# Kernel optimization log

Hardware: AMD Instinct MI355X
Metric: run time of the kernel (lower is better)

The kernel has to match this reference:

```python
import jax, jax.numpy as jnp
import numpy as np

B, H, W, C = 128, 56, 56, 96
N = H * W  # tokens


def setup_inputs() -> dict:
    key = jax.random.key(0)
    k1, k2 = jax.random.split(key)
    x = jax.random.normal(k1, (B, N, C), dtype=jnp.float32)
    # original inits to 0.02 * ones; use small random values for a non-trivial baseline
    weight_c = jax.random.uniform(k2, (N, C // 2 + 1, 2), dtype=jnp.float32) * 0.02
    return {"x": x, "weight_c": weight_c}


def reference(x, weight_c):
    # x: [B, N, C]; rfft along channel dim, per-token complex filter, irfft back
    c = x.shape[2]
    xf = jnp.fft.rfft(x.astype(jnp.float32), axis=2, norm="ortho")  # [B, N, C//2+1] complex
    w = jax.lax.complex(weight_c[..., 0], weight_c[..., 1])          # [N, C//2+1] complex
    y = xf * w  # broadcast over batch
    return jnp.fft.irfft(y, n=c, axis=2, norm="ortho")  # [B, N, C]
```

## Files before the change

kernel.cpp:

```cpp
#include <hip/hip_runtime.h>
#include <hip/hip_bf16.h>

#ifndef M_PI
#define M_PI 3.14159265358979323846
#endif

static constexpr int B_ = 128;
static constexpr int N_ = 3136;
static constexpr int C_ = 96;
static constexpr int PITCH = 104;

typedef short short8 __attribute__((ext_vector_type(8)));
typedef float float4v __attribute__((ext_vector_type(4)));

static __device__ __forceinline__ unsigned short f2bf(float f) {
  __hip_bfloat16 b = __float2bfloat16(f);
  return *reinterpret_cast<unsigned short*>(&b);
}

__global__ __launch_bounds__(256, 3) void gf_mfma_kernel(
    const float* __restrict__ x, const float* __restrict__ wc,
    float* __restrict__ y) {
  const int n = blockIdx.x;
  const int tid = threadIdx.x;

  __shared__ __align__(16) unsigned short Asm[128 * PITCH];
  __shared__ __align__(16) unsigned short Ht[96 * PITCH];
  __shared__ float wsh[98];
  __shared__ float cs[96];
  __shared__ float sn[96];
  __shared__ unsigned short hrevd[192];

  float4 xv[12];
  const float* xbase = x + (size_t)n * C_;
#pragma unroll
  for (int p = 0; p < 12; ++p) {
    const int fidx = p * 256 + tid;
    const int b = fidx / 24;
    const int t4 = fidx - b * 24;
    xv[p] = *reinterpret_cast<const float4*>(xbase + (size_t)b * (N_ * C_) + 4 * t4);
  }

  if (tid < 98) wsh[tid] = wc[n * 98 + tid];
  if (tid < 96) {
    float s, c;
    sincosf((float)(2.0 * M_PI / 96.0) * (float)tid, &s, &c);
    cs[tid] = c;
    sn[tid] = s;
  }
  __syncthreads();

  if (tid < 96) {
    const int c = tid;
    float acc = wsh[0] + ((c & 1) ? -wsh[96] : wsh[96]);
    int idx = c;
    for (int k = 1; k <= 47; ++k) {
      acc += 2.0f * (wsh[2 * k] * cs[idx] - wsh[2 * k + 1] * sn[idx]);
      idx += c;
      if (idx >= 96) idx -= 96;
    }
    const unsigned short hb = f2bf(acc * (1.0f / 96.0f));
    hrevd[96 - c] = hb;
    hrevd[(c == 0) ? 0 : (192 - c)] = hb;
  }

#pragma unroll
  for (int p = 0; p < 12; ++p) {
    const int fidx = p * 256 + tid;
    const int b = fidx / 24;
    const int t4 = fidx - b * 24;
    ushort4 o;
    o.x = f2bf(xv[p].x);
    o.y = f2bf(xv[p].y);
    o.z = f2bf(xv[p].z);
    o.w = f2bf(xv[p].w);
    *reinterpret_cast<ushort4*>(&Asm[b * PITCH + 4 * t4]) = o;
  }
  __syncthreads();

  for (int j = tid; j < 96 * 48; j += 256) {
    const int c = j / 48;
    const int kp = j - c * 48;
    const int m = 96 - c + 2 * kp;
    const unsigned int lo = hrevd[m];
    const unsigned int hi = hrevd[m + 1];
    *reinterpret_cast<unsigned int*>(&Ht[c * PITCH + 2 * kp]) = lo | (hi << 16);
  }
  __syncthreads();

  const int wv = tid >> 6;
  const int l = tid & 63;
  const int lrow = l & 15;
  const int lk = l >> 4;

  float4v acc[2][6];
#pragma unroll
  for (int mt = 0; mt < 2; ++mt)
#pragma unroll
    for (int nt = 0; nt < 6; ++nt)
#pragma unroll
      for (int i = 0; i < 4; ++i) acc[mt][nt][i] = 0.0f;

  short8 afr[2][3];
#pragma unroll
  for (int mt = 0; mt < 2; ++mt)
#pragma unroll
    for (int kq = 0; kq < 3; ++kq)
      afr[mt][kq] = *reinterpret_cast<const short8*>(
          &Asm[((wv * 2 + mt) * 16 + lrow) * PITCH + kq * 32 + lk * 8]);

#pragma unroll
  for (int nt = 0; nt < 6; ++nt) {
#pragma unroll
    for (int kq = 0; kq < 3; ++kq) {
      const short8 bfr = *reinterpret_cast<const short8*>(
          &Ht[(nt * 16 + lrow) * PITCH + kq * 32 + lk * 8]);
      acc[0][nt] = __builtin_amdgcn_mfma_f32_16x16x32_bf16(afr[0][kq], bfr, acc[0][nt], 0, 0, 0);
      acc[1][nt] = __builtin_amdgcn_mfma_f32_16x16x32_bf16(afr[1][kq], bfr, acc[1][nt], 0, 0, 0);
    }
  }

#pragma unroll
  for (int mt = 0; mt < 2; ++mt) {
    const int brow0 = (wv * 2 + mt) * 16 + lk * 4;
#pragma unroll
    for (int i = 0; i < 4; ++i) {
      float* yp = y + (size_t)(brow0 + i) * (N_ * C_) + (size_t)n * C_;
#pragma unroll
      for (int nt = 0; nt < 6; ++nt) {
        yp[nt * 16 + lrow] = acc[mt][nt][i];
      }
    }
  }
}

extern "C" void kernel_launch(void* const* d_in, const int* in_sizes, int n_in,
                              void* d_out, int out_size, void* d_ws, size_t ws_size,
                              hipStream_t stream) {
  const float* x = (const float*)d_in[0];
  const float* wc = (const float*)d_in[1];
  float* y = (float*)d_out;

  hipLaunchKernelGGL(gf_mfma_kernel, dim3(N_), dim3(256), 0, stream, x, wc, y);
}
```

Baseline: 284.7 us.

## Split circulant filter build into prepass kernel and drop LDS staging from GEMM

A separate kernel computes each token's bf16 circulant filter once and writes it to workspace in eight shifted copies, so the main kernel can read MFMA B fragments straight from global memory with aligned 16-byte loads. The main kernel also loads x directly into A fragments in registers instead of staging through shared memory. This removes the LDS traffic, the barriers and the per-block sincos/DFT work, and raises the occupancy hint to 4. In exchange it adds a second launch and about 9.6 MB of workspace traffic, and the old path is kept as a fallback when the workspace is too small.

```diff
diff --git a/kernel.cpp b/kernel.cpp
--- a/kernel.cpp
+++ b/kernel.cpp
@@ -8,6 +8,7 @@
 static constexpr int B_ = 128;
 static constexpr int N_ = 3136;
 static constexpr int C_ = 96;
+static constexpr int NC = N_ * C_;
 static constexpr int PITCH = 104;
 
 typedef short short8 __attribute__((ext_vector_type(8)));
@@ -16,6 +17,124 @@
 static __device__ __forceinline__ unsigned short f2bf(float f) {
   __hip_bfloat16 b = __float2bfloat16(f);
   return *reinterpret_cast<unsigned short*>(&b);
+}
+
+__global__ __launch_bounds__(128) void gf_hbuild_kernel(
+    const float* __restrict__ wc, unsigned short* __restrict__ wsB) {
+  const int n = blockIdx.x;
+  const int tid = threadIdx.x;
+  __shared__ float wsh[98];
+  __shared__ float cs[96], sn[96];
+  __shared__ unsigned short hlb[96];
+
+  if (tid < 98) wsh[tid] = wc[n * 98 + tid];
+  if (tid < 96) {
+    float s, c;
+    sincosf((float)(2.0 * M_PI / 96.0) * (float)tid, &s, &c);
+    cs[tid] = c;
+    sn[tid] = s;
+  }
+  __syncthreads();
+
+  if (tid < 96) {
+    const int c = tid;
+    float acc = wsh[0] + ((c & 1) ? -wsh[96] : wsh[96]);
+    int idx = c;
+    for (int k = 1; k <= 47; ++k) {
+      acc += 2.0f * (wsh[2 * k] * cs[idx] - wsh[2 * k + 1] * sn[idx]);
+      idx += c;
+      if (idx >= 96) idx -= 96;
+    }
+    hlb[c] = f2bf(acc * (1.0f / 96.0f));
+  }
+  __syncthreads();
+
+  unsigned int* out = reinterpret_cast<unsigned int*>(wsB + (size_t)n * 1536);
+  for (int e = tid; e < 768; e += 128) {
+    const int s = e / 96;
+    const int jp = e - s * 96;
+    const int a = 288 - (2 * jp + s);
+    const unsigned int lo = hlb[a % 96];
+    const unsigned int hi = hlb[(a - 1) % 96];
+    out[e] = lo | (hi << 16);
+  }
+}
+
+__global__ __launch_bounds__(256, 4) void gf_mfma2_kernel(
+    const float* __restrict__ x, const unsigned short* __restrict__ wsB,
+    float* __restrict__ y) {
+  const int n = blockIdx.x;
+  const int tid = threadIdx.x;
+  const int wv = tid >> 6;
+  const int l = tid & 63;
+  const int lrow = l & 15;
+  const int lk = l >> 4;
+
+  float4 v0[2][3], v1[2][3];
+#pragma unroll
+  for (int mt = 0; mt < 2; ++mt) {
+    const float* xp =
+        x + (size_t)((wv * 2 + mt) * 16 + lrow) * NC + n * C_ + lk * 8;
+#pragma unroll
+    for (int kq = 0; kq < 3; ++kq) {
+      v0[mt][kq] = *reinterpret_cast<const float4*>(xp + kq * 32);
+      v1[mt][kq] = *reinterpret_cast<const float4*>(xp + kq * 32 + 4);
+    }
+  }
+  short8 afr[2][3];
+#pragma unroll
+  for (int mt = 0; mt < 2; ++mt)
+#pragma unroll
+    for (int kq = 0; kq < 3; ++kq) {
+      short8 a;
+      a[0] = (short)f2bf(v0[mt][kq].x);
+      a[1] = (short)f2bf(v0[mt][kq].y);
+      a[2] = (short)f2bf(v0[mt][kq].z);
+      a[3] = (short)f2bf(v0[mt][kq].w);
+      a[4] = (short)f2bf(v1[mt][kq].x);
+      a[5] = (short)f2bf(v1[mt][kq].y);
+      a[6] = (short)f2bf(v1[mt][kq].z);
+      a[7] = (short)f2bf(v1[mt][kq].w);
+      afr[mt][kq] = a;
+    }
+
+  const int M0 = 96 + lk * 8 - lrow;
+  const unsigned short* wb0 =
+      wsB + (size_t)n * 1536 + (M0 & 7) * 192 + (M0 & ~7);
+
+  float4v acc[2][6];
+#pragma unroll
+  for (int mt = 0; mt < 2; ++mt)
+#pragma unroll
+    for (int nt = 0; nt < 6; ++nt)
+#pragma unroll
+      for (int i = 0; i < 4; ++i) acc[mt][nt][i] = 0.0f;
+
+#pragma unroll
+  for (int nt = 0; nt < 6; ++nt) {
+#pragma unroll
+    for (int kq = 0; kq < 3; ++kq) {
+      const short8 bfr =
+          *reinterpret_cast<const short8*>(wb0 + kq * 32 - nt * 16);
+      acc[0][nt] = __builtin_amdgcn_mfma_f32_16x16x32_bf16(afr[0][kq], bfr,
+                                                           acc[0][nt], 0, 0, 0);
+      acc[1][nt] = __builtin_amdgcn_mfma_f32_16x16x32_bf16(afr[1][kq], bfr,
+                                                           acc[1][nt], 0, 0, 0);
+    }
+  }
+
+#pragma unroll
+  for (int mt = 0; mt < 2; ++mt) {
+    const int brow0 = (wv * 2 + mt) * 16 + lk * 4;
+#pragma unroll
+    for (int i = 0; i < 4; ++i) {
+      float* yp = y + (size_t)(brow0 + i) * NC + (size_t)n * C_;
+#pragma unroll
+      for (int nt = 0; nt < 6; ++nt) {
+        yp[nt * 16 + lrow] = acc[mt][nt][i];
+      }
+    }
+  }
 }
 
 __global__ __launch_bounds__(256, 3) void gf_mfma_kernel(
@@ -38,7 +157,7 @@
     const int fidx = p * 256 + tid;
     const int b = fidx / 24;
     const int t4 = fidx - b * 24;
-    xv[p] = *reinterpret_cast<const float4*>(xbase + (size_t)b * (N_ * C_) + 4 * t4);
+    xv[p] = *reinterpret_cast<const float4*>(xbase + (size_t)b * NC + 4 * t4);
   }
 
   if (tid < 98) wsh[tid] = wc[n * 98 + tid];
@@ -115,8 +234,10 @@
     for (int kq = 0; kq < 3; ++kq) {
       const short8 bfr = *reinterpret_cast<const short8*>(
           &Ht[(nt * 16 + lrow) * PITCH + kq * 32 + lk * 8]);
-      acc[0][nt] = __builtin_amdgcn_mfma_f32_16x16x32_bf16(afr[0][kq], bfr, acc[0][nt], 0, 0, 0);
-      acc[1][nt] = __builtin_amdgcn_mfma_f32_16x16x32_bf16(afr[1][kq], bfr, acc[1][nt], 0, 0, 0);
+      acc[0][nt] = __builtin_amdgcn_mfma_f32_16x16x32_bf16(afr[0][kq], bfr,
+                                                           acc[0][nt], 0, 0, 0);
+      acc[1][nt] = __builtin_amdgcn_mfma_f32_16x16x32_bf16(afr[1][kq], bfr,
+                                                           acc[1][nt], 0, 0, 0);
     }
   }
 
@@ -125,7 +246,7 @@
     const int brow0 = (wv * 2 + mt) * 16 + lk * 4;
 #pragma unroll
     for (int i = 0; i < 4; ++i) {
-      float* yp = y + (size_t)(brow0 + i) * (N_ * C_) + (size_t)n * C_;
+      float* yp = y + (size_t)(brow0 + i) * NC + (size_t)n * C_;
 #pragma unroll
       for (int nt = 0; nt < 6; ++nt) {
         yp[nt * 16 + lrow] = acc[mt][nt][i];
@@ -141,5 +262,12 @@
   const float* wc = (const float*)d_in[1];
   float* y = (float*)d_out;
 
-  hipLaunchKernelGGL(gf_mfma_kernel, dim3(N_), dim3(256), 0, stream, x, wc, y);
-}
+  const size_t need = (size_t)N_ * 1536 * sizeof(unsigned short);
+  if (ws_size >= need) {
+    unsigned short* wsB = (unsigned short*)d_ws;
+    hipLaunchKernelGGL(gf_hbuild_kernel, dim3(N_), dim3(128), 0, stream, wc, wsB);
+    hipLaunchKernelGGL(gf_mfma2_kernel, dim3(N_), dim3(256), 0, stream, x, wsB, y);
+  } else {
+    hipLaunchKernelGGL(gf_mfma_kernel, dim3(N_), dim3(256), 0, stream, x, wc, y);
+  }
+}
```

After: 298.5 us. 4.8% more time.

## Load x straight into MFMA fragments and read circulant filter from compact replicated table

Applied to the files above, without the earlier changes.

Each lane now loads x directly into its MFMA operand layout and converts to bf16 in registers, which removes the shared-memory staging of x. Operands are swapped so the circulant filter is the A operand and x is B. The filter is read from a small 8-way shifted replica table instead of a materialized 96x96 matrix. Output becomes contiguous float4 stores per lane, and the filter DFT is split across 192 threads. Shared memory drops sharply, so occupancy is raised to 4 blocks per SM. The risks are more scattered global loads for x and harder-to-verify index arithmetic.

```diff
diff --git a/kernel.cpp b/kernel.cpp
--- a/kernel.cpp
+++ b/kernel.cpp
@@ -8,7 +8,7 @@
 static constexpr int B_ = 128;
 static constexpr int N_ = 3136;
 static constexpr int C_ = 96;
-static constexpr int PITCH = 104;
+static constexpr int NC = N_ * C_;
 
 typedef short short8 __attribute__((ext_vector_type(8)));
 typedef float float4v __attribute__((ext_vector_type(4)));
@@ -18,27 +18,35 @@
   return *reinterpret_cast<unsigned short*>(&b);
 }
 
-__global__ __launch_bounds__(256, 3) void gf_mfma_kernel(
+static __device__ __forceinline__ int mod96(int a) {
+  return a >= 192 ? a - 192 : (a >= 96 ? a - 96 : a);
+}
+
+__global__ __launch_bounds__(256, 4) void gf_fused_kernel(
     const float* __restrict__ x, const float* __restrict__ wc,
     float* __restrict__ y) {
   const int n = blockIdx.x;
   const int tid = threadIdx.x;
+  const int wv = tid >> 6;
+  const int l = tid & 63;
+  const int lrow = l & 15;
+  const int lk = l >> 4;
 
-  __shared__ __align__(16) unsigned short Asm[128 * PITCH];
-  __shared__ __align__(16) unsigned short Ht[96 * PITCH];
   __shared__ float wsh[98];
-  __shared__ float cs[96];
-  __shared__ float sn[96];
-  __shared__ unsigned short hrevd[192];
+  __shared__ float cs[96], sn[96];
+  __shared__ float hpart[2][96];
+  __shared__ __align__(16) unsigned short hrep[1536];
 
-  float4 xv[12];
-  const float* xbase = x + (size_t)n * C_;
+  float4 v0[2][3], v1[2][3];
 #pragma unroll
-  for (int p = 0; p < 12; ++p) {
-    const int fidx = p * 256 + tid;
-    const int b = fidx / 24;
-    const int t4 = fidx - b * 24;
-    xv[p] = *reinterpret_cast<const float4*>(xbase + (size_t)b * (N_ * C_) + 4 * t4);
+  for (int bt = 0; bt < 2; ++bt) {
+    const float* xp =
+        x + (size_t)((wv * 2 + bt) * 16 + lrow) * NC + n * C_ + lk * 8;
+#pragma unroll
+    for (int kq = 0; kq < 3; ++kq) {
+      v0[bt][kq] = *reinterpret_cast<const float4*>(xp + kq * 32);
+      v1[bt][kq] = *reinterpret_cast<const float4*>(xp + kq * 32 + 4);
+    }
   }
 
   if (tid < 98) wsh[tid] = wc[n * 98 + tid];
@@ -50,86 +58,98 @@
   }
   __syncthreads();
 
-  if (tid < 96) {
-    const int c = tid;
-    float acc = wsh[0] + ((c & 1) ? -wsh[96] : wsh[96]);
-    int idx = c;
-    for (int k = 1; k <= 47; ++k) {
+  if (tid < 192) {
+    const int half = (tid >= 96) ? 1 : 0;
+    const int c = tid - half * 96;
+    float acc;
+    int idx, k0, k1;
+    if (half == 0) {
+      acc = wsh[0] + ((c & 1) ? -wsh[96] : wsh[96]);
+      idx = c;
+      k0 = 1; k1 = 24;
+    } else {
+      acc = 0.0f;
+      int m0 = 24 * (c & 3) + c;
+      if (m0 >= 96) m0 -= 96;
+      idx = m0;
+      k0 = 25; k1 = 47;
+    }
+    for (int k = k0; k <= k1; ++k) {
       acc += 2.0f * (wsh[2 * k] * cs[idx] - wsh[2 * k + 1] * sn[idx]);
       idx += c;
       if (idx >= 96) idx -= 96;
     }
-    const unsigned short hb = f2bf(acc * (1.0f / 96.0f));
-    hrevd[96 - c] = hb;
-    hrevd[(c == 0) ? 0 : (192 - c)] = hb;
-  }
-
-#pragma unroll
-  for (int p = 0; p < 12; ++p) {
-    const int fidx = p * 256 + tid;
-    const int b = fidx / 24;
-    const int t4 = fidx - b * 24;
-    ushort4 o;
-    o.x = f2bf(xv[p].x);
-    o.y = f2bf(xv[p].y);
-    o.z = f2bf(xv[p].z);
-    o.w = f2bf(xv[p].w);
-    *reinterpret_cast<ushort4*>(&Asm[b * PITCH + 4 * t4]) = o;
+    hpart[half][c] = acc;
   }
   __syncthreads();
 
-  for (int j = tid; j < 96 * 48; j += 256) {
-    const int c = j / 48;
-    const int kp = j - c * 48;
-    const int m = 96 - c + 2 * kp;
-    const unsigned int lo = hrevd[m];
-    const unsigned int hi = hrevd[m + 1];
-    *reinterpret_cast<unsigned int*>(&Ht[c * PITCH + 2 * kp]) = lo | (hi << 16);
+  {
+    unsigned int* out = reinterpret_cast<unsigned int*>(hrep);
+#pragma unroll
+    for (int r = 0; r < 3; ++r) {
+      const int e = r * 256 + tid;
+      const int s = e / 96;
+      const int jp = e - s * 96;
+      const int a = 288 - (2 * jp + s);
+      const int i0 = mod96(a);
+      const int i1 = mod96(a - 1);
+      const unsigned int lo =
+          f2bf((hpart[0][i0] + hpart[1][i0]) * (1.0f / 96.0f));
+      const unsigned int hi =
+          f2bf((hpart[0][i1] + hpart[1][i1]) * (1.0f / 96.0f));
+      out[e] = lo | (hi << 16);
+    }
   }
+
+  short8 xfr[2][3];
+#pragma unroll
+  for (int bt = 0; bt < 2; ++bt)
+#pragma unroll
+    for (int kq = 0; kq < 3; ++kq) {
+      short8 a;
+      a[0] = (short)f2bf(v0[bt][kq].x);
+      a[1] = (short)f2bf(v0[bt][kq].y);
+      a[2] = (short)f2bf(v0[bt][kq].z);
+      a[3] = (short)f2bf(v0[bt][kq].w);
+      a[4] = (short)f2bf(v1[bt][kq].x);
+      a[5] = (short)f2bf(v1[bt][kq].y);
+      a[6] = (short)f2bf(v1[bt][kq].z);
+      a[7] = (short)f2bf(v1[bt][kq].w);
+      xfr[bt][kq] = a;
+    }
   __syncthreads();
 
-  const int wv = tid >> 6;
-  const int l = tid & 63;
-  const int lrow = l & 15;
-  const int lk = l >> 4;
+  const int M0 = 96 + lk * 8 - lrow;
+  const unsigned short* wb0 = hrep + (M0 & 7) * 192 + (M0 & ~7);
 
   float4v acc[2][6];
 #pragma unroll
-  for (int mt = 0; mt < 2; ++mt)
+  for (int bt = 0; bt < 2; ++bt)
 #pragma unroll
     for (int nt = 0; nt < 6; ++nt)
 #pragma unroll
-      for (int i = 0; i < 4; ++i) acc[mt][nt][i] = 0.0f;
-
-  short8 afr[2][3];
-#pragma unroll
-  for (int mt = 0; mt < 2; ++mt)
-#pragma unroll
-    for (int kq = 0; kq < 3; ++kq)
-      afr[mt][kq] = *reinterpret_cast<const short8*>(
-          &Asm[((wv * 2 + mt) * 16 + lrow) * PITCH + kq * 32 + lk * 8]);
+      for (int i = 0; i < 4; ++i) acc[bt][nt][i] = 0.0f;
 
 #pragma unroll
   for (int nt = 0; nt < 6; ++nt) {
 #pragma unroll
     for (int kq = 0; kq < 3; ++kq) {
-      const short8 bfr = *reinterpret_cast<const short8*>(
-          &Ht[(nt * 16 + lrow) * PITCH + kq * 32 + lk * 8]);
-      acc[0][nt] = __builtin_amdgcn_mfma_f32_16x16x32_bf16(afr[0][kq], bfr, acc[0][nt], 0, 0, 0);
-      acc[1][nt] = __builtin_amdgcn_mfma_f32_16x16x32_bf16(afr[1][kq], bfr, acc[1][nt], 0, 0, 0);
+      const short8 hfr =
+          *reinterpret_cast<const short8*>(wb0 + kq * 32 - nt * 16);
+      acc[0][nt] = __builtin_amdgcn_mfma_f32_16x16x32_bf16(hfr, xfr[0][kq],
+                                                           acc[0][nt], 0, 0, 0);
+      acc[1][nt] = __builtin_amdgcn_mfma_f32_16x16x32_bf16(hfr, xfr[1][kq],
+                                                           acc[1][nt], 0, 0, 0);
     }
   }
 
 #pragma unroll
-  for (int mt = 0; mt < 2; ++mt) {
-    const int brow0 = (wv * 2 + mt) * 16 + lk * 4;
+  for (int bt = 0; bt < 2; ++bt) {
+    float* yp = y + (size_t)((wv * 2 + bt) * 16 + lrow) * NC +
+                (size_t)n * C_ + lk * 4;
 #pragma unroll
-    for (int i = 0; i < 4; ++i) {
-      float* yp = y + (size_t)(brow0 + i) * (N_ * C_) + (size_t)n * C_;
-#pragma unroll
-      for (int nt = 0; nt < 6; ++nt) {
-        yp[nt * 16 + lrow] = acc[mt][nt][i];
-      }
+    for (int nt = 0; nt < 6; ++nt) {
+      *reinterpret_cast<float4v*>(yp + nt * 16) = acc[bt][nt];
     }
   }
 }
@@ -141,5 +161,5 @@
   const float* wc = (const float*)d_in[1];
   float* y = (float*)d_out;
 
-  hipLaunchKernelGGL(gf_mfma_kernel, dim3(N_), dim3(256), 0, stream, x, wc, y);
+  hipLaunchKernelGGL(gf_fused_kernel, dim3(N_), dim3(256), 0, stream, x, wc, y);
 }
```

After: 286.0 us. About the same (+0.4%).
